# Kernel optimization log

Measured on AMD Instinct MI355X. Metric: run time of the kernel, lower is better.

## Reference

```python
import jax, jax.numpy as jnp
import numpy as np

BETA = 0.25  # commitment cost
EPS = 1e-10


def _vq_layer(xf, cb):
    # xf: [M, D] flattened features, cb: [K, D] codebook
    K = cb.shape[0]
    M = xf.shape[0]
    d = (jnp.sum(xf * xf, axis=-1, keepdims=True)
         - 2.0 * (xf @ cb.T)
         + jnp.sum(cb * cb, axis=-1))
    idx = jnp.argmin(d, axis=-1)          # [M]
    q = cb[idx]                           # [M, D]
    # commitment + codebook loss (VQ-VAE)
    commit = jnp.mean((jax.lax.stop_gradient(q) - xf) ** 2)
    cbloss = jnp.mean((q - jax.lax.stop_gradient(xf)) ** 2)
    loss = cbloss + BETA * commit
    # straight-through estimator
    q_st = xf + jax.lax.stop_gradient(q - xf)
    # codebook usage perplexity
    counts = jnp.zeros((K,), dtype=xf.dtype).at[idx].add(1.0)
    p = counts / M
    perplexity = jnp.exp(-jnp.sum(p * jnp.log(p + EPS)))
    return q_st, idx, loss, perplexity


def setup_inputs() -> dict:
    key = jax.random.key(0)
    k1, k2 = jax.random.split(key)
    B, N, D, H, W, K = 32, 4, 128, 32, 32, 1024
    x = jax.random.normal(k1, (B, N * D, H, W), dtype=jnp.float32)
    codebooks = jax.random.normal(k2, (N, K, D), dtype=jnp.float32)
    return {"x": x, "codebooks": codebooks}


def reference(x, codebooks):
    B, C, H, W = x.shape
    N, K, D = codebooks.shape
    assert C == N * D
    M = B * H * W
    # [B, N*D, H, W] -> [N, M, D]
    xs = x.reshape(B, N, D, H, W).transpose(1, 0, 3, 4, 2).reshape(N, M, D)
    q, idx, loss, perp = jax.vmap(_vq_layer)(xs, codebooks)
    # quantized_cat: [N, M, D] -> [B, N*D, H, W]  (cat along channel dim)
    quantized_cat = (q.reshape(N, B, H, W, D)
                      .transpose(1, 0, 4, 2, 3)
                      .reshape(B, N * D, H, W))
    # indices_cat: [N, M] -> [B, N, H, W]
    indices_cat = idx.reshape(N, B, H, W).transpose(1, 0, 2, 3)
    return quantized_cat, indices_cat, loss, perp
```

## Files before the change

### kernel.cpp

```cpp
#include <hip/hip_runtime.h>

#define B_ 32
#define N_ 4
#define D_ 128
#define M_ 32768
#define K_ 1024

#define IDX_OFF 16777216
#define LOSS_OFF 16908288
#define PERP_OFF 16908292

#define WS_LOSS 0
#define WS_CNT 1024
#define WS_ENORM 8192
#define WS_BPACK_F 16384
#define BPACK_LAYER_US 262144

#define SBIAS 384.0f
#define MARGIN 0.012f

typedef __bf16 bf16x8 __attribute__((ext_vector_type(8)));
typedef float f32x4 __attribute__((ext_vector_type(4)));

union FragU {
  bf16x8 v;
  ushort u16[8];
  uint4 q;
};

__device__ __forceinline__ ushort bf16_hi_rne(float f, float* hif) {
  uint u = __float_as_uint(f);
  uint r = (u + 0x7fffu + ((u >> 16) & 1u)) >> 16;
  *hif = __uint_as_float(r << 16);
  return (ushort)r;
}
__device__ __forceinline__ ushort bf16_rne(float f) {
  uint u = __float_as_uint(f);
  return (ushort)((u + 0x7fffu + ((u >> 16) & 1u)) >> 16);
}

__device__ __forceinline__ void gload_lds16(const void* g, void* l) {
  __builtin_amdgcn_global_load_lds(
      (const __attribute__((address_space(1))) unsigned int*)g,
      (__attribute__((address_space(3))) unsigned int*)l, 16, 0, 0);
}

__global__ void vq_pack(const float* __restrict__ cb, float* __restrict__ ws) {
  int blk = blockIdx.x, tid = threadIdx.x;
  if (blk < 256) {
    int n = blk >> 6, tile = blk & 63;
    int s = tid >> 6, lane = tid & 63;
    int code = tile * 16 + (lane & 15);
    int dbase = s * 32 + ((lane >> 4) << 3);
    const float* src = cb + ((size_t)(n * K_ + code)) * D_ + dbase;
    float4 v0 = *(const float4*)src;
    float4 v1 = *(const float4*)(src + 4);
    float v[8] = {v0.x, v0.y, v0.z, v0.w, v1.x, v1.y, v1.z, v1.w};
    FragU fh, fl;
#pragma unroll
    for (int j = 0; j < 8; ++j) {
      float hif;
      fh.u16[j] = bf16_hi_rne(v[j], &hif);
      fl.u16[j] = bf16_rne(v[j] - hif);
    }
    ushort* base = (ushort*)(ws + WS_BPACK_F) + (size_t)n * BPACK_LAYER_US +
                   ((size_t)(tile * 4 + s) * 2) * 512 + lane * 8;
    *(uint4*)base = fh.q;
    *(uint4*)(base + 512) = fl.q;
  } else if (blk < 1280) {
    int lane = tid & 63, w = tid >> 6;
    int waveid = (blk - 256) * 4 + w;
    int n = waveid >> 10, k = waveid & 1023;
    const float2* row = (const float2*)(cb + (size_t)(n * K_ + k) * D_);
    float2 v = row[lane];
    float ss = fmaf(v.x, v.x, v.y * v.y);
#pragma unroll
    for (int off = 32; off; off >>= 1) ss += __shfl_down(ss, off, 64);
    if (lane == 0) ws[WS_ENORM + n * K_ + k] = SBIAS - 0.5f * ss;
  } else {
#pragma unroll
    for (int i = 0; i < 20; ++i) ws[i * 256 + tid] = 0.f;
  }
}

__global__ __launch_bounds__(256, 4) void vq_main(const float* __restrict__ x,
                                                  const float* __restrict__ cb,
                                                  float* __restrict__ ws,
                                                  float* __restrict__ out) {
  __shared__ alignas(16) ushort Bsm[18432];
  const int tid = threadIdx.x;
  const int bid = blockIdx.x;
  const int n = bid >> 8;
  const int mblk = bid & 255;
  const int b = mblk >> 3;
  const int hw0 = (mblk & 7) << 7;

  const int lane = tid & 63, w = tid >> 6;
  const int quad = lane >> 4, l15 = lane & 15;

  const float* xbase = x + (size_t)((b * 4 + n) * 128) * 1024 + hw0;
  const float* cbn = cb + (size_t)n * K_ * D_;
  const float* enB = ws + WS_ENORM + n * K_;
  const ushort* bpack_n = (ushort*)(ws + WS_BPACK_F) + (size_t)n * BPACK_LAYER_US;

  char* ext = (char*)Bsm + 32768;
  int* sIdx = (int*)ext;
  float* dist = (float*)(ext + 512);
  int* list = (int*)(ext + 1024);
  int* lcnt = (int*)(ext + 1536);
  double* xrowd = (double*)(ext + 1544);
  double* rd = (double*)(ext + 2568);
  int* rk = (int*)(ext + 2600);

  if (tid == 0) *lcnt = 0;

  bf16x8 ahi[2][4], alo[2][4];
#pragma unroll
  for (int set = 0; set < 2; ++set) {
    const int hwl = w * 32 + set * 16 + l15;
    float xs = 0.f;
#pragma unroll
    for (int s = 0; s < 4; ++s) {
      const int dbase = s * 32 + quad * 8;
      FragU fh, fl;
#pragma unroll
      for (int j = 0; j < 8; ++j) {
        float v = xbase[(size_t)(dbase + j) * 1024 + hwl];
        xs = fmaf(v, v, xs);
        float hif;
        fh.u16[j] = bf16_hi_rne(v, &hif);
        fl.u16[j] = bf16_rne(v - hif);
      }
      ahi[set][s] = fh.v;
      alo[set][s] = fl.v;
    }
    xs += __shfl_xor(xs, 16, 64);
    xs += __shfl_xor(xs, 32, 64);
    if (l15 == lane) dist[w * 32 + set * 16 + l15] = xs;
  }

  uint best[8], best2[8];
#pragma unroll
  for (int i = 0; i < 8; ++i) { best[i] = 0u; best2[i] = 0u; }

  const uint4* gsrc = (const uint4*)bpack_n;
  uint4* Bsm4 = (uint4*)Bsm;

#pragma unroll
  for (int i = 0; i < 4; ++i)
    gload_lds16(gsrc + i * 256 + w * 64 + lane, Bsm4 + i * 256 + w * 64);

#pragma unroll 1
  for (int c = 0; c < 32; ++c) {
    __syncthreads();
    if (c < 31) {
      const uint4* src = gsrc + (c + 1) * 1024;
      uint4* dst = Bsm4 + ((c + 1) & 1) * 1024;
#pragma unroll
      for (int i = 0; i < 4; ++i)
        gload_lds16(src + i * 256 + w * 64 + lane, dst + i * 256 + w * 64);
    }
    const ushort* Bcur = Bsm + (c & 1) * 8192;
#pragma unroll
    for (int tin = 0; tin < 2; ++tin) {
      const int t = c * 2 + tin;
      const uint tinv = (uint)(63 - t);
      float en = enB[t * 16 + l15];
      bf16x8 bh[4], bl[4];
#pragma unroll
      for (int s = 0; s < 4; ++s) {
        const ushort* p = Bcur + ((tin * 4 + s) * 2) * 512 + lane * 8;
        bh[s] = ((const FragU*)p)->v;
        bl[s] = ((const FragU*)(p + 512))->v;
      }
      f32x4 acc[2];
#pragma unroll
      for (int set = 0; set < 2; ++set) acc[set] = (f32x4){0.f, 0.f, 0.f, 0.f};
#pragma unroll
      for (int s = 0; s < 4; ++s) {
#pragma unroll
        for (int set = 0; set < 2; ++set)
          acc[set] = __builtin_amdgcn_mfma_f32_16x16x32_bf16(ahi[set][s], bh[s], acc[set], 0, 0, 0);
#pragma unroll
        for (int set = 0; set < 2; ++set)
          acc[set] = __builtin_amdgcn_mfma_f32_16x16x32_bf16(ahi[set][s], bl[s], acc[set], 0, 0, 0);
#pragma unroll
        for (int set = 0; set < 2; ++set)
          acc[set] = __builtin_amdgcn_mfma_f32_16x16x32_bf16(alo[set][s], bh[s], acc[set], 0, 0, 0);
      }
#pragma unroll
      for (int set = 0; set < 2; ++set) {
#pragma unroll
        for (int r = 0; r < 4; ++r) {
          float sb = acc[set][r] + en;
          uint key = (__float_as_uint(sb) & 0xFFFFFFC0u) | tinv;
          uint ob = best[set * 4 + r];
          uint mn = key < ob ? key : ob;
          best[set * 4 + r] = key > ob ? key : ob;
          if (mn > best2[set * 4 + r]) best2[set * 4 + r] = mn;
        }
      }
    }
  }
  __syncthreads();

  uint* sS = (uint*)Bsm;
  uint* sS2 = (uint*)((char*)Bsm + 8704);
#pragma unroll
  for (int set = 0; set < 2; ++set) {
#pragma unroll
    for (int r = 0; r < 4; ++r) {
      int m = w * 32 + set * 16 + quad * 4 + r;
      sS[m * 17 + l15] = best[set * 4 + r];
      sS2[m * 17 + l15] = best2[set * 4 + r];
    }
  }
  __syncthreads();

  if (tid < 128) {
    int m = tid;
    uint g1 = 0, g2 = 0;
    int gi = 0;
#pragma unroll 4
    for (int li = 0; li < 16; ++li) {
      uint key = sS[m * 17 + li];
      uint sb = key >> 6;
      int kk = (int)(63u - (key & 63u)) * 16 + li;
      if (sb > g1) { g2 = g1; g1 = sb; gi = kk; }
      else {
        if (sb == g1 && kk < gi) gi = kk;
        if (sb > g2) g2 = sb;
      }
      uint sb2 = sS2[m * 17 + li] >> 6;
      if (sb2 > g2) g2 = sb2;
    }
    sIdx[m] = gi;
    float s1f = __uint_as_float(g1 << 6);
    dist[m] = dist[m] - 2.0f * (s1f - SBIAS);
    float gap = s1f - __uint_as_float(g2 << 6);
    if (gap < MARGIN) {
      int pos = atomicAdd(lcnt, 1);
      list[pos] = m;
    }
  }
  __syncthreads();

  const int cnt = *lcnt;
  for (int i = 0; i < cnt; ++i) {
    const int m = list[i];
    if (tid < 128) xrowd[tid] = (double)xbase[(size_t)tid * 1024 + m];
    __syncthreads();
    double bd = 1e300;
    int bk = 0;
#pragma unroll 1
    for (int j = 0; j < 4; ++j) {
      const int k = tid * 4 + j;
      const float4* er = (const float4*)(cbn + (size_t)k * D_);
      double d = 0.0;
#pragma unroll 8
      for (int c4 = 0; c4 < 32; ++c4) {
        float4 e = er[c4];
        double d0 = xrowd[c4 * 4 + 0] - (double)e.x;
        double d1 = xrowd[c4 * 4 + 1] - (double)e.y;
        double d2 = xrowd[c4 * 4 + 2] - (double)e.z;
        double d3 = xrowd[c4 * 4 + 3] - (double)e.w;
        d = fma(d0, d0, d);
        d = fma(d1, d1, d);
        d = fma(d2, d2, d);
        d = fma(d3, d3, d);
      }
      if (d < bd) { bd = d; bk = k; }
    }
#pragma unroll
    for (int off = 32; off; off >>= 1) {
      double od = __shfl_down(bd, off, 64);
      int ok = __shfl_down(bk, off, 64);
      if (od < bd || (od == bd && ok < bk)) { bd = od; bk = ok; }
    }
    if (lane == 0) { rd[w] = bd; rk[w] = bk; }
    __syncthreads();
    if (tid == 0) {
      double gb = rd[0];
      int gk = rk[0];
      for (int t = 1; t < 4; ++t)
        if (rd[t] < gb || (rd[t] == gb && rk[t] < gk)) { gb = rd[t]; gk = rk[t]; }
      sIdx[m] = gk;
      dist[m] = (float)gb;
    }
    __syncthreads();
  }

  if (tid < 128) {
    int bi = sIdx[tid];
    out[IDX_OFF + (b * 4 + n) * 1024 + hw0 + tid] = (float)bi;
    atomicAdd(ws + WS_CNT + n * K_ + bi, 1.0f);
  }
  float lp = (tid < 128) ? dist[tid] : 0.f;
#pragma unroll
  for (int off = 32; off; off >>= 1) lp += __shfl_down(lp, off, 64);
  if (lane == 0 && w < 2) atomicAdd(ws + WS_LOSS + n, lp);
  __syncthreads();

  float* Qs = (float*)Bsm;
  float* out0 = out + (size_t)((b * 4 + n) * 128) * 1024 + hw0;
#pragma unroll 1
  for (int h = 0; h < 2; ++h) {
    const int m = tid & 127, part = tid >> 7;
    const float* src = cbn + (size_t)sIdx[m] * D_ + h * 64 + part * 32;
#pragma unroll
    for (int i = 0; i < 8; ++i) {
      float4 v = ((const float4*)src)[i];
      int dl = part * 32 + i * 4;
      Qs[(dl + 0) * 128 + m] = v.x;
      Qs[(dl + 1) * 128 + m] = v.y;
      Qs[(dl + 2) * 128 + m] = v.z;
      Qs[(dl + 3) * 128 + m] = v.w;
    }
    __syncthreads();
#pragma unroll
    for (int it = 0; it < 8; ++it) {
      int e = it * 256 + tid;
      int m4 = (e & 31) * 4;
      int dl = e >> 5;
      float4 v = *(float4*)(Qs + dl * 128 + m4);
      *(float4*)(out0 + (size_t)(h * 64 + dl) * 1024 + m4) = v;
    }
    __syncthreads();
  }
}

__global__ void vq_finalize(const float* __restrict__ ws, float* __restrict__ out) {
  int n = blockIdx.x;
  int t = threadIdx.x;
  const float* counts = ws + WS_CNT + n * K_;
  float s = 0.f;
  for (int k = t; k < K_; k += 256) {
    float p = counts[k] * (1.0f / 32768.0f);
    s += p * logf(p + 1e-10f);
  }
  __shared__ float red[4];
#pragma unroll
  for (int off = 32; off; off >>= 1) s += __shfl_down(s, off, 64);
  if ((t & 63) == 0) red[t >> 6] = s;
  __syncthreads();
  if (t == 0) {
    s = red[0] + red[1] + red[2] + red[3];
    out[PERP_OFF + n] = expf(-s);
    out[LOSS_OFF + n] = 1.25f * ws[WS_LOSS + n] / 4194304.0f;
  }
}

extern "C" void kernel_launch(void* const* d_in, const int* in_sizes, int n_in,
                              void* d_out, int out_size, void* d_ws, size_t ws_size,
                              hipStream_t stream) {
  const float* x = (const float*)d_in[0];
  const float* cb = (const float*)d_in[1];
  float* out = (float*)d_out;
  float* ws = (float*)d_ws;
  vq_pack<<<1281, 256, 0, stream>>>(cb, ws);
  vq_main<<<1024, 256, 0, stream>>>(x, cb, ws, out);
  vq_finalize<<<4, 256, 0, stream>>>(ws, out);
}
```

Baseline: 281.7 us.

## Replace split-bf16 triple MFMA with single fp16 MFMA and batch exact rescoring

Result: faster. 252.5 us (-10.4%).

```diff
diff --git a/kernel.cpp b/kernel.cpp
--- a/kernel.cpp
+++ b/kernel.cpp
@@ -14,30 +14,20 @@
 #define WS_CNT 1024
 #define WS_ENORM 8192
 #define WS_BPACK_F 16384
-#define BPACK_LAYER_US 262144
+#define BPACK_LAYER_US 131072
 
 #define SBIAS 384.0f
-#define MARGIN 0.012f
-
-typedef __bf16 bf16x8 __attribute__((ext_vector_type(8)));
+#define MARGIN 0.04f
+
+typedef _Float16 f16x8 __attribute__((ext_vector_type(8)));
 typedef float f32x4 __attribute__((ext_vector_type(4)));
 
-union FragU {
-  bf16x8 v;
+union FragH {
+  f16x8 v;
+  _Float16 h[8];
   ushort u16[8];
   uint4 q;
 };
-
-__device__ __forceinline__ ushort bf16_hi_rne(float f, float* hif) {
-  uint u = __float_as_uint(f);
-  uint r = (u + 0x7fffu + ((u >> 16) & 1u)) >> 16;
-  *hif = __uint_as_float(r << 16);
-  return (ushort)r;
-}
-__device__ __forceinline__ ushort bf16_rne(float f) {
-  uint u = __float_as_uint(f);
-  return (ushort)((u + 0x7fffu + ((u >> 16) & 1u)) >> 16);
-}
 
 __device__ __forceinline__ void gload_lds16(const void* g, void* l) {
   __builtin_amdgcn_global_load_lds(
@@ -56,17 +46,12 @@
     float4 v0 = *(const float4*)src;
     float4 v1 = *(const float4*)(src + 4);
     float v[8] = {v0.x, v0.y, v0.z, v0.w, v1.x, v1.y, v1.z, v1.w};
-    FragU fh, fl;
-#pragma unroll
-    for (int j = 0; j < 8; ++j) {
-      float hif;
-      fh.u16[j] = bf16_hi_rne(v[j], &hif);
-      fl.u16[j] = bf16_rne(v[j] - hif);
-    }
+    FragH f;
+#pragma unroll
+    for (int j = 0; j < 8; ++j) f.h[j] = (_Float16)v[j];
     ushort* base = (ushort*)(ws + WS_BPACK_F) + (size_t)n * BPACK_LAYER_US +
-                   ((size_t)(tile * 4 + s) * 2) * 512 + lane * 8;
-    *(uint4*)base = fh.q;
-    *(uint4*)(base + 512) = fl.q;
+                   (size_t)(tile * 4 + s) * 512 + lane * 8;
+    *(uint4*)base = f.q;
   } else if (blk < 1280) {
     int lane = tid & 63, w = tid >> 6;
     int waveid = (blk - 256) * 4 + w;
@@ -108,13 +93,10 @@
   float* dist = (float*)(ext + 512);
   int* list = (int*)(ext + 1024);
   int* lcnt = (int*)(ext + 1536);
-  double* xrowd = (double*)(ext + 1544);
-  double* rd = (double*)(ext + 2568);
-  int* rk = (int*)(ext + 2600);
 
   if (tid == 0) *lcnt = 0;
 
-  bf16x8 ahi[2][4], alo[2][4];
+  f16x8 ah[2][4];
 #pragma unroll
   for (int set = 0; set < 2; ++set) {
     const int hwl = w * 32 + set * 16 + l15;
@@ -122,17 +104,14 @@
 #pragma unroll
     for (int s = 0; s < 4; ++s) {
       const int dbase = s * 32 + quad * 8;
-      FragU fh, fl;
+      FragH fh;
 #pragma unroll
       for (int j = 0; j < 8; ++j) {
         float v = xbase[(size_t)(dbase + j) * 1024 + hwl];
         xs = fmaf(v, v, xs);
-        float hif;
-        fh.u16[j] = bf16_hi_rne(v, &hif);
-        fl.u16[j] = bf16_rne(v - hif);
-      }
-      ahi[set][s] = fh.v;
-      alo[set][s] = fl.v;
+        fh.h[j] = (_Float16)v;
+      }
+      ah[set][s] = fh.v;
     }
     xs += __shfl_xor(xs, 16, 64);
     xs += __shfl_xor(xs, 32, 64);
@@ -151,9 +130,9 @@
     gload_lds16(gsrc + i * 256 + w * 64 + lane, Bsm4 + i * 256 + w * 64);
 
 #pragma unroll 1
-  for (int c = 0; c < 32; ++c) {
+  for (int c = 0; c < 16; ++c) {
     __syncthreads();
-    if (c < 31) {
+    if (c < 15) {
       const uint4* src = gsrc + (c + 1) * 1024;
       uint4* dst = Bsm4 + ((c + 1) & 1) * 1024;
 #pragma unroll
@@ -162,16 +141,15 @@
     }
     const ushort* Bcur = Bsm + (c & 1) * 8192;
 #pragma unroll
-    for (int tin = 0; tin < 2; ++tin) {
-      const int t = c * 2 + tin;
+    for (int tin = 0; tin < 4; ++tin) {
+      const int t = c * 4 + tin;
       const uint tinv = (uint)(63 - t);
       float en = enB[t * 16 + l15];
-      bf16x8 bh[4], bl[4];
+      f16x8 bv[4];
 #pragma unroll
       for (int s = 0; s < 4; ++s) {
-        const ushort* p = Bcur + ((tin * 4 + s) * 2) * 512 + lane * 8;
-        bh[s] = ((const FragU*)p)->v;
-        bl[s] = ((const FragU*)(p + 512))->v;
+        const ushort* p = Bcur + (tin * 4 + s) * 512 + lane * 8;
+        bv[s] = ((const FragH*)p)->v;
       }
       f32x4 acc[2];
 #pragma unroll
@@ -180,13 +158,7 @@
       for (int s = 0; s < 4; ++s) {
 #pragma unroll
         for (int set = 0; set < 2; ++set)
-          acc[set] = __builtin_amdgcn_mfma_f32_16x16x32_bf16(ahi[set][s], bh[s], acc[set], 0, 0, 0);
-#pragma unroll
-        for (int set = 0; set < 2; ++set)
-          acc[set] = __builtin_amdgcn_mfma_f32_16x16x32_bf16(ahi[set][s], bl[s], acc[set], 0, 0, 0);
-#pragma unroll
-        for (int set = 0; set < 2; ++set)
-          acc[set] = __builtin_amdgcn_mfma_f32_16x16x32_bf16(alo[set][s], bh[s], acc[set], 0, 0, 0);
+          acc[set] = __builtin_amdgcn_mfma_f32_16x16x32_f16(ah[set][s], bv[s], acc[set], 0, 0, 0);
       }
 #pragma unroll
       for (int set = 0; set < 2; ++set) {
@@ -246,48 +218,74 @@
   __syncthreads();
 
   const int cnt = *lcnt;
-  for (int i = 0; i < cnt; ++i) {
-    const int m = list[i];
-    if (tid < 128) xrowd[tid] = (double)xbase[(size_t)tid * 1024 + m];
-    __syncthreads();
-    double bd = 1e300;
-    int bk = 0;
+  if (cnt > 0) {
+    char* rbase = (char*)Bsm;
+    float* xrs = (float*)rbase;
+    double* dred = (double*)(rbase + 2048);
+    int* kred = (int*)(rbase + 3072);
+    const int g = tid >> 3, h = tid & 7;
+    for (int g0 = 0; g0 < cnt; g0 += 4) {
+      const int R = (cnt - g0 < 4) ? (cnt - g0) : 4;
+      for (int e = tid; e < R * 128; e += 256) {
+        int r = e >> 7, d = e & 127;
+        xrs[e] = xbase[(size_t)d * 1024 + list[g0 + r]];
+      }
+      __syncthreads();
+      double pbd[4];
+      int pbk[4];
+#pragma unroll
+      for (int r = 0; r < 4; ++r) { pbd[r] = 1e300; pbk[r] = 0; }
 #pragma unroll 1
-    for (int j = 0; j < 4; ++j) {
-      const int k = tid * 4 + j;
-      const float4* er = (const float4*)(cbn + (size_t)k * D_);
-      double d = 0.0;
-#pragma unroll 8
-      for (int c4 = 0; c4 < 32; ++c4) {
-        float4 e = er[c4];
-        double d0 = xrowd[c4 * 4 + 0] - (double)e.x;
-        double d1 = xrowd[c4 * 4 + 1] - (double)e.y;
-        double d2 = xrowd[c4 * 4 + 2] - (double)e.z;
-        double d3 = xrowd[c4 * 4 + 3] - (double)e.w;
-        d = fma(d0, d0, d);
-        d = fma(d1, d1, d);
-        d = fma(d2, d2, d);
-        d = fma(d3, d3, d);
-      }
-      if (d < bd) { bd = d; bk = k; }
-    }
-#pragma unroll
-    for (int off = 32; off; off >>= 1) {
-      double od = __shfl_down(bd, off, 64);
-      int ok = __shfl_down(bk, off, 64);
-      if (od < bd || (od == bd && ok < bk)) { bd = od; bk = ok; }
-    }
-    if (lane == 0) { rd[w] = bd; rk[w] = bk; }
-    __syncthreads();
-    if (tid == 0) {
-      double gb = rd[0];
-      int gk = rk[0];
-      for (int t = 1; t < 4; ++t)
-        if (rd[t] < gb || (rd[t] == gb && rk[t] < gk)) { gb = rd[t]; gk = rk[t]; }
-      sIdx[m] = gk;
-      dist[m] = (float)gb;
-    }
-    __syncthreads();
+      for (int c = 0; c < 32; ++c) {
+        const int k = c * 32 + g;
+        const float4* er = (const float4*)(cbn + (size_t)k * D_) + h * 4;
+        float4 E0 = er[0], E1 = er[1], E2 = er[2], E3 = er[3];
+#pragma unroll
+        for (int r = 0; r < 4; ++r) {
+          if (r < R) {
+            const float4* xp4 = (const float4*)(xrs + r * 128) + h * 4;
+            double pd = 0.0;
+            float4 xv;
+            xv = xp4[0];
+            { double d0=(double)xv.x-E0.x, d1=(double)xv.y-E0.y, d2=(double)xv.z-E0.z, d3=(double)xv.w-E0.w;
+              pd=fma(d0,d0,pd); pd=fma(d1,d1,pd); pd=fma(d2,d2,pd); pd=fma(d3,d3,pd); }
+            xv = xp4[1];
+            { double d0=(double)xv.x-E1.x, d1=(double)xv.y-E1.y, d2=(double)xv.z-E1.z, d3=(double)xv.w-E1.w;
+              pd=fma(d0,d0,pd); pd=fma(d1,d1,pd); pd=fma(d2,d2,pd); pd=fma(d3,d3,pd); }
+            xv = xp4[2];
+            { double d0=(double)xv.x-E2.x, d1=(double)xv.y-E2.y, d2=(double)xv.z-E2.z, d3=(double)xv.w-E2.w;
+              pd=fma(d0,d0,pd); pd=fma(d1,d1,pd); pd=fma(d2,d2,pd); pd=fma(d3,d3,pd); }
+            xv = xp4[3];
+            { double d0=(double)xv.x-E3.x, d1=(double)xv.y-E3.y, d2=(double)xv.z-E3.z, d3=(double)xv.w-E3.w;
+              pd=fma(d0,d0,pd); pd=fma(d1,d1,pd); pd=fma(d2,d2,pd); pd=fma(d3,d3,pd); }
+            pd += __shfl_xor(pd, 1, 64);
+            pd += __shfl_xor(pd, 2, 64);
+            pd += __shfl_xor(pd, 4, 64);
+            if (pd < pbd[r]) { pbd[r] = pd; pbk[r] = k; }
+          }
+        }
+      }
+      if (h == 0) {
+#pragma unroll
+        for (int r = 0; r < 4; ++r)
+          if (r < R) { dred[r * 32 + g] = pbd[r]; kred[r * 32 + g] = pbk[r]; }
+      }
+      __syncthreads();
+      if (tid < R) {
+        double bd = 1e300;
+        int bk = 0;
+#pragma unroll 4
+        for (int g2 = 0; g2 < 32; ++g2) {
+          double d = dred[tid * 32 + g2];
+          int kk = kred[tid * 32 + g2];
+          if (d < bd || (d == bd && kk < bk)) { bd = d; bk = kk; }
+        }
+        int m = list[g0 + tid];
+        sIdx[m] = bk;
+        dist[m] = (float)bd;
+      }
+      __syncthreads();
+    }
   }
 
   if (tid < 128) {
```
